# Kernel tuning notes

Measured on AMD Instinct MI355X. Metric: run time of the kernel, lower is better.

## Reference

```python
import jax, jax.numpy as jnp
import numpy as np

B, S, D = 8, 1024, 768
H, HD = 12, 64  # heads, head dim (H*HD == D)
EPS = 1e-12


def setup_inputs() -> dict:
    key = jax.random.key(0)
    ks = jax.random.split(key, 8)
    s = 0.02
    return {
        "hidden_states": jax.random.normal(ks[0], (B, S, D), jnp.float32),
        "attention_mask": jnp.zeros((B, 1, 1, S), jnp.float32),
        "head_mask": jnp.ones((H,), jnp.float32),
        "Wq": jax.random.normal(ks[1], (D, H * HD), jnp.float32) * s,
        "bq": jnp.zeros((H * HD,), jnp.float32),
        "Wk": jax.random.normal(ks[2], (D, H * HD), jnp.float32) * s,
        "bk": jnp.zeros((H * HD,), jnp.float32),
        "Wv": jax.random.normal(ks[3], (D, H * HD), jnp.float32) * s,
        "bv": jnp.zeros((H * HD,), jnp.float32),
        "Wo": jax.random.normal(ks[4], (D, H * HD), jnp.float32) * s,  # torch Linear weight [out=D, in=H*HD]
        "bo": jnp.zeros((D,), jnp.float32),
        "gamma": jnp.ones((D,), jnp.float32),
        "beta": jnp.zeros((D,), jnp.float32),
    }


def reference(hidden_states, attention_mask, head_mask, Wq, bq, Wk, bk, Wv, bv, Wo, bo, gamma, beta):
    def heads(x):  # [B,S,H*HD] -> [B,H,S,HD]
        return x.reshape(B, S, H, HD).transpose(0, 2, 1, 3)

    q = heads(hidden_states @ Wq.T + bq)
    k = heads(hidden_states @ Wk.T + bk)
    v = heads(hidden_states @ Wv.T + bv)

    scores = jnp.einsum("bhqd,bhkd->bhqk", q, k) / np.sqrt(HD).astype(np.float32)
    scores = scores + attention_mask
    probs = jax.nn.softmax(scores, axis=-1)  # dropout p=0 (eval)
    ctx = jnp.einsum("bhqk,bhkd->bhqd", probs, v)  # [B,H,S,HD]

    # masked per-head output projection: Wo.T.view(H, HD, D)
    Wph = Wo.T.reshape(H, HD, D)
    proj = jnp.einsum("bhsd,hde,h->bse", ctx, Wph, head_mask) + bo

    # residual + LayerNorm
    x = proj + hidden_states
    mu = jnp.mean(x, axis=-1, keepdims=True)
    var = jnp.mean(jnp.square(x - mu), axis=-1, keepdims=True)
    out = (x - mu) * jax.lax.rsqrt(var + EPS) * gamma + beta
    return out
```

## Files before the change

kernel.cpp:

```cpp
#include <hip/hip_runtime.h>
#include <hip/hip_bf16.h>
#include <math.h>

#define Bn 8
#define Sn 1024
#define Dn 768
#define Hn 12
#define MROWS (Bn * Sn)

typedef __attribute__((ext_vector_type(8))) short short8;
typedef __attribute__((ext_vector_type(4))) float floatx4;

__device__ __forceinline__ unsigned short f2b(float x) {
    union { float f; unsigned u; } v; v.f = x;
    unsigned r = v.u + 0x7fffu + ((v.u >> 16) & 1u);
    return (unsigned short)(r >> 16);
}

__device__ __forceinline__ unsigned pk2(float a, float b) {
    union { __hip_bfloat162 h; unsigned u; } v;
    v.h = __float22bfloat162_rn(float2{a, b});
    return v.u;
}

__device__ __forceinline__ float fexp2(float x) {
    float r;
    asm("v_exp_f32 %0, %1" : "=v"(r) : "v"(x));
    return r;
}

__device__ __forceinline__ void gload16(const void* g, void* l) {
    __builtin_amdgcn_global_load_lds(
        (const __attribute__((address_space(1))) void*)g,
        (__attribute__((address_space(3))) void*)l, 16, 0, 0);
}

#define MEMFENCE() asm volatile("" ::: "memory")
#define WAITV3()  asm volatile("s_waitcnt vmcnt(3)" ::: "memory")
#define WAITV0()  asm volatile("s_waitcnt vmcnt(0)" ::: "memory")
#define WAITLGKM() asm volatile("s_waitcnt lgkmcnt(0)" ::: "memory")


__global__ __launch_bounds__(256) void convert_all(const float* __restrict__ X,
                                                   const float* __restrict__ Wq, const float* __restrict__ Wk,
                                                   const float* __restrict__ Wv, const float* __restrict__ Wo,
                                                   unsigned short* __restrict__ Xb,
                                                   unsigned short* __restrict__ Wqb, unsigned short* __restrict__ Wkb,
                                                   unsigned short* __restrict__ Wvb, unsigned short* __restrict__ Wob) {
    const int id = blockIdx.x;
    const float* src;
    unsigned short* dst;
    int i;
    if (id < 6144) {
        src = X; dst = Xb;
        i = id * 256 + threadIdx.x;
    } else {
        const int y = (id - 6144) / 576;
        src = (y == 0) ? Wq : (y == 1) ? Wk : (y == 2) ? Wv : Wo;
        dst = (y == 0) ? Wqb : (y == 1) ? Wkb : (y == 2) ? Wvb : Wob;
        i = ((id - 6144) % 576) * 256 + threadIdx.x;
    }
    float4 v = reinterpret_cast<const float4*>(src)[i];
    ushort4 o;
    o.x = f2b(v.x); o.y = f2b(v.y); o.z = f2b(v.z); o.w = f2b(v.w);
    reinterpret_cast<ushort4*>(dst)[i] = o;
}

#define QKV_STAGE(t, b)                                                        \
    {                                                                          \
        const int k0 = (t) * 32;                                               \
        gload16(gAsrc[0] + k0, lAdst[0] + (b) * 8192);                         \
        gload16(gAsrc[1] + k0, lAdst[1] + (b) * 8192);                         \
        gload16(gWsrc + k0, lWdst + (b) * 4096);                               \
    }

#define QKV_COMP(b)                                                            \
    {                                                                          \
        const unsigned short* Ab = &As[b][0];                                  \
        const unsigned short* Wb = &Ws[b][0];                                  \
        short8 bf[4];                                                          \
        _Pragma("unroll") for (int j = 0; j < 4; j++)                          \
            bf[j] = *(const short8*)&Wb[woff[j]];                              \
        __builtin_amdgcn_s_setprio(1);                                         \
        _Pragma("unroll") for (int i = 0; i < 4; i++) {                        \
            short8 af = *(const short8*)&Ab[aoff[i]];                          \
            _Pragma("unroll") for (int j = 0; j < 4; j++)                      \
                acc[i][j] = __builtin_amdgcn_mfma_f32_16x16x32_bf16(           \
                    af, bf[j], acc[i][j], 0, 0, 0);                            \
        }                                                                      \
        __builtin_amdgcn_s_setprio(0);                                         \
    }

__global__ __launch_bounds__(512, 4) void gemm_qkv(const unsigned short* __restrict__ A,
                                                   const unsigned short* __restrict__ Wq,
                                                   const unsigned short* __restrict__ Wk,
                                                   const unsigned short* __restrict__ Wv,
                                                   const float* __restrict__ bq,
                                                   const float* __restrict__ bk,
                                                   const float* __restrict__ bv,
                                                   unsigned short* __restrict__ Qh,
                                                   unsigned short* __restrict__ Kh,
                                                   unsigned short* __restrict__ Vt) {
    __shared__ __align__(16) unsigned short As[3][256 * 32];
    __shared__ __align__(16) unsigned short Ws[3][128 * 32];
    const int orig = blockIdx.x;
    const int chunk = orig & 7;
    const int local = orig >> 3;
    const int by = chunk * 4 + local / 18;
    const int bxr = local % 18;
    const int mat = bxr / 6;
    const int m0 = by * 256;
    const int n0 = (bxr % 6) * 128;
    const unsigned short* W = (mat == 0) ? Wq : (mat == 1) ? Wk : Wv;
    const float* bias = (mat == 0) ? bq : (mat == 1) ? bk : bv;
    unsigned short* Cout = (mat == 0) ? Qh : (mat == 1) ? Kh : Vt;

    const int tid = threadIdx.x;
    const int w = tid >> 6, l = tid & 63, quad = l >> 4, mr = l & 15;
    const int wm = (w >> 1) * 64;
    const int wn = (w & 1) * 64;

    const unsigned short* gAsrc[2];
    unsigned short* lAdst[2];
#pragma unroll
    for (int j = 0; j < 2; j++) {
        const int u = tid + j * 512;
        const int r = u >> 2, c = u & 3;
        const int cp = c ^ ((r >> 1) & 3);
        gAsrc[j] = &A[(size_t)(m0 + r) * Dn + cp * 8];
        lAdst[j] = &As[0][u * 8];
    }
    const unsigned short* gWsrc;
    unsigned short* lWdst;
    {
        const int u = tid;
        const int r = u >> 2, c = u & 3;
        const int cp = c ^ ((r >> 1) & 3);
        gWsrc = &W[(size_t)(n0 + r) * Dn + cp * 8];
        lWdst = &Ws[0][u * 8];
    }

    int aoff[4], woff[4];
#pragma unroll
    for (int i = 0; i < 4; i++) {
        const int ra = wm + i * 16 + mr;
        aoff[i] = (ra * 4 + (quad ^ ((ra >> 1) & 3))) * 8;
    }
#pragma unroll
    for (int j = 0; j < 4; j++) {
        const int rw = wn + j * 16 + mr;
        woff[j] = (rw * 4 + (quad ^ ((rw >> 1) & 3))) * 8;
    }

    floatx4 acc[4][4];
#pragma unroll
    for (int i = 0; i < 4; i++)
#pragma unroll
        for (int j = 0; j < 4; j++) {
            floatx4 z = {0.f, 0.f, 0.f, 0.f};
            acc[i][j] = z;
        }

    QKV_STAGE(0, 0);
    QKV_STAGE(1, 1);

    for (int t = 0; t < 21; t += 3) {
        WAITV3();
        __builtin_amdgcn_s_barrier();
        MEMFENCE();
        QKV_STAGE(t + 2, 2);
        QKV_COMP(0);

        WAITV3();
        __builtin_amdgcn_s_barrier();
        MEMFENCE();
        QKV_STAGE(t + 3, 0);
        QKV_COMP(1);

        WAITV3();
        __builtin_amdgcn_s_barrier();
        MEMFENCE();
        QKV_STAGE(t + 4, 1);
        QKV_COMP(2);
    }
    WAITV3();
    __builtin_amdgcn_s_barrier();
    MEMFENCE();
    QKV_STAGE(23, 2);
    QKV_COMP(0);

    WAITV3();
    __builtin_amdgcn_s_barrier();
    MEMFENCE();
    QKV_COMP(1);

    WAITV0();
    __builtin_amdgcn_s_barrier();
    MEMFENCE();
    QKV_COMP(2);

#pragma unroll
    for (int j = 0; j < 4; j++) {
        const int col = n0 + wn + j * 16 + mr;
        const float bval = bias[col];
        const int h = col >> 6, d = col & 63;
#pragma unroll
        for (int i = 0; i < 4; i++) {
            const int mbase = m0 + wm + i * 16 + quad * 4;
            const int b = mbase >> 10, s0 = mbase & 1023;
            const size_t base = (size_t)(b * Hn + h) << 16;
            if (mat == 2) {
                ushort4 o;
                o.x = f2b(acc[i][j][0] + bval);
                o.y = f2b(acc[i][j][1] + bval);
                o.z = f2b(acc[i][j][2] + bval);
                o.w = f2b(acc[i][j][3] + bval);
                *reinterpret_cast<ushort4*>(&Cout[base + (size_t)d * 1024 + s0]) = o;
            } else {
#pragma unroll
                for (int r = 0; r < 4; r++) {
                    const float val = acc[i][j][r] + bval;
                    Cout[base + (size_t)(s0 + r) * 64 + d] = f2b(val);
                }
            }
        }
    }
}

#define OUT_STAGE(t, b)                                                        \
    {                                                                          \
        const int k0 = (t) * 32;                                               \
        gload16(gAsrc + k0, lAdst + (b) * 2048);                               \
        gload16(gWsrc[0] + k0, lWdst[0] + (b) * 4096);                         \
        gload16(gWsrc[1] + k0, lWdst[1] + (b) * 4096);                         \
    }

#define OUT_COMP(b)                                                            \
    {                                                                          \
        const unsigned short* Ab = &As[b][0];                                  \
        const unsigned short* Wb = &Ws[b][0];                                  \
        short8 bf[2];                                                          \
        _Pragma("unroll") for (int j = 0; j < 2; j++)                          \
            bf[j] = *(const short8*)&Wb[woff[j]];                              \
        __builtin_amdgcn_s_setprio(1);                                         \
        _Pragma("unroll") for (int i = 0; i < 4; i++) {                        \
            short8 af = *(const short8*)&Ab[aoff[i]];                          \
            _Pragma("unroll") for (int j = 0; j < 2; j++)                      \
                acc[i][j] = __builtin_amdgcn_mfma_f32_16x16x32_bf16(           \
                    af, bf[j], acc[i][j], 0, 0, 0);                            \
        }                                                                      \
        __builtin_amdgcn_s_setprio(0);                                         \
    }

__global__ __launch_bounds__(256, 4) void gemm_out(const unsigned short* __restrict__ A,
                                                   const unsigned short* __restrict__ W,
                                                   const float* __restrict__ bias,
                                                   const float* __restrict__ X,
                                                   float* __restrict__ xres) {
    __shared__ __align__(16) unsigned short As[3][64 * 32];
    __shared__ __align__(16) unsigned short Ws[3][128 * 32];
    const int id = blockIdx.x;
    const int by = id & 127;
    const int bx = id >> 7;
    const int m0 = by * 64;
    const int n0 = bx * 128;

    const int tid = threadIdx.x;
    const int w = tid >> 6, l = tid & 63, quad = l >> 4, mr = l & 15;

    const unsigned short* gAsrc;
    unsigned short* lAdst;
    {
        const int u = tid;
        const int r = u >> 2, c = u & 3;
        const int cp = c ^ ((r >> 1) & 3);
        gAsrc = &A[(size_t)(m0 + r) * Dn + cp * 8];
        lAdst = &As[0][u * 8];
    }
    const unsigned short* gWsrc[2];
    unsigned short* lWdst[2];
#pragma unroll
    for (int j = 0; j < 2; j++) {
        const int u = tid + j * 256;
        const int r = u >> 2, c = u & 3;
        const int cp = c ^ ((r >> 1) & 3);
        gWsrc[j] = &W[(size_t)(n0 + r) * Dn + cp * 8];
        lWdst[j] = &Ws[0][u * 8];
    }

    int aoff[4], woff[2];
#pragma unroll
    for (int i = 0; i < 4; i++) {
        const int ra = i * 16 + mr;
        aoff[i] = (ra * 4 + (quad ^ ((ra >> 1) & 3))) * 8;
    }
#pragma unroll
    for (int j = 0; j < 2; j++) {
        const int rw = w * 32 + j * 16 + mr;
        woff[j] = (rw * 4 + (quad ^ ((rw >> 1) & 3))) * 8;
    }

    floatx4 acc[4][2];
#pragma unroll
    for (int i = 0; i < 4; i++)
#pragma unroll
        for (int j = 0; j < 2; j++) {
            floatx4 z = {0.f, 0.f, 0.f, 0.f};
            acc[i][j] = z;
        }

    OUT_STAGE(0, 0);
    OUT_STAGE(1, 1);

    for (int t = 0; t < 21; t += 3) {
        WAITV3();
        __builtin_amdgcn_s_barrier();
        MEMFENCE();
        OUT_STAGE(t + 2, 2);
        OUT_COMP(0);

        WAITV3();
        __builtin_amdgcn_s_barrier();
        MEMFENCE();
        OUT_STAGE(t + 3, 0);
        OUT_COMP(1);

        WAITV3();
        __builtin_amdgcn_s_barrier();
        MEMFENCE();
        OUT_STAGE(t + 4, 1);
        OUT_COMP(2);
    }
    WAITV3();
    __builtin_amdgcn_s_barrier();
    MEMFENCE();
    OUT_STAGE(23, 2);
    OUT_COMP(0);

    WAITV3();
    __builtin_amdgcn_s_barrier();
    MEMFENCE();
    OUT_COMP(1);

    WAITV0();
    __builtin_amdgcn_s_barrier();
    MEMFENCE();
    OUT_COMP(2);

#pragma unroll
    for (int j = 0; j < 2; j++) {
        const int col = n0 + w * 32 + j * 16 + mr;
        const float bval = bias[col];
#pragma unroll
        for (int i = 0; i < 4; i++) {
#pragma unroll
            for (int r = 0; r < 4; r++) {
                const int m = m0 + i * 16 + quad * 4 + r;
                xres[(size_t)m * Dn + col] = acc[i][j][r] + bval + X[(size_t)m * Dn + col];
            }
        }
    }
}

__global__ __launch_bounds__(256) void flash_attn_mfma(const unsigned short* __restrict__ Qh,
                                                       const unsigned short* __restrict__ Kh,
                                                       const unsigned short* __restrict__ Vt,
                                                       const float* __restrict__ mask,
                                                       const float* __restrict__ head_mask,
                                                       unsigned short* __restrict__ ctx) {
    __shared__ __align__(16) unsigned short Ks[64 * 72];
    __shared__ __align__(16) unsigned short Vs[64 * 72];
    __shared__ __align__(16) unsigned short Ps[128 * 72];
    __shared__ float msk[64];

    const float LOG2E = 1.44269504088896f;
    const float C1 = 0.125f * 1.44269504088896f;

    const int id = blockIdx.x;
    const int bh = id % 96;
    const int qt = id / 96;
    const int b = bh / Hn, h = bh % Hn;
    const int q0 = qt * 128;
    const int tid = threadIdx.x;
    const int w = tid >> 6, l = tid & 63, quad = l >> 4, mr = l & 15;
    const size_t hb = (size_t)(b * Hn + h) << 16;

    short8 aq[2][2];
#pragma unroll
    for (int j = 0; j < 2; j++)
#pragma unroll
        for (int ks = 0; ks < 2; ks++)
            aq[j][ks] = *(const short8*)&Qh[hb + (size_t)(q0 + w * 32 + j * 16 + mr) * 64 + ks * 32 + quad * 8];

    float l_s[2] = {0.f, 0.f};
    floatx4 oacc[2][4];
#pragma unroll
    for (int i = 0; i < 2; i++)
#pragma unroll
        for (int jj = 0; jj < 4; jj++) {
            floatx4 z = {0.f, 0.f, 0.f, 0.f};
            oacc[i][jj] = z;
        }

    const int srow = tid >> 2;
    const int scol = (tid & 3) * 16;

    short8 pk0 = *(const short8*)&Kh[hb + (size_t)srow * 64 + scol];
    short8 pk1 = *(const short8*)&Kh[hb + (size_t)srow * 64 + scol + 8];
    short8 pv0 = *(const short8*)&Vt[hb + (size_t)srow * 1024 + scol];
    short8 pv1 = *(const short8*)&Vt[hb + (size_t)srow * 1024 + scol + 8];
    float pm = mask[b * Sn + (tid & 63)];

    for (int kt = 0; kt < Sn / 64; kt++) {
        __builtin_amdgcn_s_barrier();
        MEMFENCE();
        *(short8*)&Ks[srow * 72 + scol] = pk0;
        *(short8*)&Ks[srow * 72 + scol + 8] = pk1;
        *(short8*)&Vs[srow * 72 + scol] = pv0;
        *(short8*)&Vs[srow * 72 + scol + 8] = pv1;
        if (tid < 64) msk[tid] = pm * LOG2E;
        if (kt < Sn / 64 - 1) {
            const int k0 = (kt + 1) * 64;
            pk0 = *(const short8*)&Kh[hb + (size_t)(k0 + srow) * 64 + scol];
            pk1 = *(const short8*)&Kh[hb + (size_t)(k0 + srow) * 64 + scol + 8];
            pv0 = *(const short8*)&Vt[hb + (size_t)srow * 1024 + k0 + scol];
            pv1 = *(const short8*)&Vt[hb + (size_t)srow * 1024 + k0 + scol + 8];
            pm = mask[b * Sn + k0 + (tid & 63)];
        }
        WAITLGKM();
        __builtin_amdgcn_s_barrier();
        MEMFENCE();

        floatx4 sacc[4][2];
#pragma unroll
        for (int i = 0; i < 4; i++)
#pragma unroll
            for (int j = 0; j < 2; j++) {
                floatx4 z = {0.f, 0.f, 0.f, 0.f};
                sacc[i][j] = z;
            }
#pragma unroll
        for (int ks = 0; ks < 2; ks++) {
            short8 kfr[4];
#pragma unroll
            for (int i = 0; i < 4; i++)
                kfr[i] = *(const short8*)&Ks[(i * 16 + mr) * 72 + ks * 32 + quad * 8];
            __builtin_amdgcn_s_setprio(1);
#pragma unroll
            for (int i = 0; i < 4; i++)
#pragma unroll
                for (int j = 0; j < 2; j++)
                    sacc[i][j] = __builtin_amdgcn_mfma_f32_16x16x32_bf16(kfr[i], aq[j][ks], sacc[i][j], 0, 0, 0);
            __builtin_amdgcn_s_setprio(0);
        }

#pragma unroll
        for (int i = 0; i < 4; i++) {
            floatx4 mk4 = *(const floatx4*)&msk[i * 16 + quad * 4];
#pragma unroll
            for (int j = 0; j < 2; j++) {
                float p[4];
#pragma unroll
                for (int r = 0; r < 4; r++) {
                    p[r] = fexp2(sacc[i][j][r] * C1 + mk4[r]);
                    l_s[j] += p[r];
                }
                uint2 w2;
                w2.x = pk2(p[0], p[1]);
                w2.y = pk2(p[2], p[3]);
                *(uint2*)&Ps[(w * 32 + j * 16 + mr) * 72 + i * 16 + quad * 4] = w2;
            }
        }

#pragma unroll
        for (int ks = 0; ks < 2; ks++) {
            short8 ap0 = *(const short8*)&Ps[(w * 32 + mr) * 72 + ks * 32 + quad * 8];
            short8 ap1 = *(const short8*)&Ps[(w * 32 + 16 + mr) * 72 + ks * 32 + quad * 8];
            __builtin_amdgcn_s_setprio(1);
#pragma unroll
            for (int jj = 0; jj < 4; jj++) {
                short8 bv = *(const short8*)&Vs[(jj * 16 + mr) * 72 + ks * 32 + quad * 8];
                oacc[0][jj] = __builtin_amdgcn_mfma_f32_16x16x32_bf16(ap0, bv, oacc[0][jj], 0, 0, 0);
                oacc[1][jj] = __builtin_amdgcn_mfma_f32_16x16x32_bf16(ap1, bv, oacc[1][jj], 0, 0, 0);
            }
            __builtin_amdgcn_s_setprio(0);
        }
    }

    float L[2];
#pragma unroll
    for (int j = 0; j < 2; j++) {
        float t = l_s[j];
        t += __shfl_xor(t, 16);
        t += __shfl_xor(t, 32);
        L[j] = t;
    }
    const float hm = head_mask[h];
    float inv[2][4];
#pragma unroll
    for (int i = 0; i < 2; i++)
#pragma unroll
        for (int r = 0; r < 4; r++)
            inv[i][r] = hm / __shfl(L[i], quad * 4 + r);

#pragma unroll
    for (int i = 0; i < 2; i++)
#pragma unroll
        for (int jj = 0; jj < 4; jj++)
#pragma unroll
            for (int r = 0; r < 4; r++) {
                const int qrow = q0 + w * 32 + i * 16 + quad * 4 + r;
                ctx[(size_t)(b * Sn + qrow) * Dn + h * 64 + jj * 16 + mr] = f2b(oacc[i][jj][r] * inv[i][r]);
            }
}

__global__ __launch_bounds__(256) void ln_kernel(const float* __restrict__ x,
                                                 const float* __restrict__ gamma,
                                                 const float* __restrict__ beta,
                                                 float* __restrict__ out) {
    __shared__ float r1[4];
    __shared__ float r2[4];
    const int m = blockIdx.x;
    const int tid = threadIdx.x;
    const int w = tid >> 6, lane = tid & 63;

    float xv[3];
    float s = 0.f, ss = 0.f;
#pragma unroll
    for (int i = 0; i < 3; i++) {
        int j = tid + i * 256;
        float t = x[(size_t)m * Dn + j];
        xv[i] = t;
        s += t;
        ss += t * t;
    }
#pragma unroll
    for (int o = 1; o < 64; o <<= 1) {
        s += __shfl_xor(s, o);
        ss += __shfl_xor(ss, o);
    }
    if (lane == 0) { r1[w] = s; r2[w] = ss; }
    __syncthreads();
    const float sum = r1[0] + r1[1] + r1[2] + r1[3];
    const float sqs = r2[0] + r2[1] + r2[2] + r2[3];
    const float mu = sum * (1.0f / Dn);
    const float var = sqs * (1.0f / Dn) - mu * mu;
    const float rstd = rsqrtf(var + 1e-12f);
#pragma unroll
    for (int i = 0; i < 3; i++) {
        int j = tid + i * 256;
        out[(size_t)m * Dn + j] = (xv[i] - mu) * rstd * gamma[j] + beta[j];
    }
}

extern "C" void kernel_launch(void* const* d_in, const int* in_sizes, int n_in,
                              void* d_out, int out_size, void* d_ws, size_t ws_size,
                              hipStream_t stream) {
    const float* X         = (const float*)d_in[0];
    const float* mask      = (const float*)d_in[1];
    const float* head_mask = (const float*)d_in[2];
    const float* Wq        = (const float*)d_in[3];
    const float* bq        = (const float*)d_in[4];
    const float* Wk        = (const float*)d_in[5];
    const float* bk        = (const float*)d_in[6];
    const float* Wv        = (const float*)d_in[7];
    const float* bv        = (const float*)d_in[8];
    const float* Wo        = (const float*)d_in[9];
    const float* bo        = (const float*)d_in[10];
    const float* gamma     = (const float*)d_in[11];
    const float* beta      = (const float*)d_in[12];
    float* out = (float*)d_out;

    const size_t NE = (size_t)Bn * Sn * Dn;
    const size_t NW = (size_t)Dn * Dn;

    char* p = (char*)d_ws;
    unsigned short* Xb  = (unsigned short*)p;  p += NE * 2;
    unsigned short* Wqb = (unsigned short*)p;  p += NW * 2;
    unsigned short* Wkb = (unsigned short*)p;  p += NW * 2;
    unsigned short* Wvb = (unsigned short*)p;  p += NW * 2;
    unsigned short* Wob = (unsigned short*)p;  p += NW * 2;
    unsigned short* Qh  = (unsigned short*)p;  p += NE * 2;
    unsigned short* Kh  = (unsigned short*)p;  p += NE * 2;
    unsigned short* Vtb = (unsigned short*)p;  p += NE * 2;
    unsigned short* ctx = (unsigned short*)p;  p += NE * 2;
    float* xres = (float*)p;

    convert_all<<<8448, 256, 0, stream>>>(X, Wq, Wk, Wv, Wo, Xb, Wqb, Wkb, Wvb, Wob);

    gemm_qkv<<<576, 512, 0, stream>>>(Xb, Wqb, Wkb, Wvb, bq, bk, bv, Qh, Kh, Vtb);

    flash_attn_mfma<<<768, 256, 0, stream>>>(Qh, Kh, Vtb, mask, head_mask, ctx);

    gemm_out<<<768, 256, 0, stream>>>(ctx, Wob, bo, X, xres);

    ln_kernel<<<MROWS, 256, 0, stream>>>(xres, gamma, beta, out);
}
```

Before: 220.9 us.

## Shrink QKV GEMM tile to 128x128 with 256-thread blocks

Changes the QKV projection GEMM from 256x128 tiles on 512-thread blocks to 128x128 tiles on 256-thread blocks, doubling the grid to 1152 blocks. It also drops the chunked block-index swizzle in favour of a plain row-major mapping, and adjusts the load staging and vmcnt waits to four loads per stage. The aim is more blocks and better wave balance across CUs, at the cost of less reuse of the weight tile per block and possibly worse L2 locality without the swizzle.

Result: no change. 216.9 us (-1.8%).

```diff
diff --git a/kernel.cpp b/kernel.cpp
--- a/kernel.cpp
+++ b/kernel.cpp
@@ -36,6 +36,7 @@
 }
 
 #define MEMFENCE() asm volatile("" ::: "memory")
+#define WAITV4()  asm volatile("s_waitcnt vmcnt(4)" ::: "memory")
 #define WAITV3()  asm volatile("s_waitcnt vmcnt(3)" ::: "memory")
 #define WAITV0()  asm volatile("s_waitcnt vmcnt(0)" ::: "memory")
 #define WAITLGKM() asm volatile("s_waitcnt lgkmcnt(0)" ::: "memory")
@@ -69,9 +70,10 @@
 #define QKV_STAGE(t, b)                                                        \
     {                                                                          \
         const int k0 = (t) * 32;                                               \
-        gload16(gAsrc[0] + k0, lAdst[0] + (b) * 8192);                         \
-        gload16(gAsrc[1] + k0, lAdst[1] + (b) * 8192);                         \
-        gload16(gWsrc + k0, lWdst + (b) * 4096);                               \
+        gload16(gAsrc[0] + k0, lAdst[0] + (b) * 4096);                         \
+        gload16(gAsrc[1] + k0, lAdst[1] + (b) * 4096);                         \
+        gload16(gWsrc[0] + k0, lWdst[0] + (b) * 4096);                         \
+        gload16(gWsrc[1] + k0, lWdst[1] + (b) * 4096);                         \
     }
 
 #define QKV_COMP(b)                                                            \
@@ -91,7 +93,7 @@
         __builtin_amdgcn_s_setprio(0);                                         \
     }
 
-__global__ __launch_bounds__(512, 4) void gemm_qkv(const unsigned short* __restrict__ A,
+__global__ __launch_bounds__(256, 3) void gemm_qkv(const unsigned short* __restrict__ A,
                                                    const unsigned short* __restrict__ Wq,
                                                    const unsigned short* __restrict__ Wk,
                                                    const unsigned short* __restrict__ Wv,
@@ -101,43 +103,35 @@
                                                    unsigned short* __restrict__ Qh,
                                                    unsigned short* __restrict__ Kh,
                                                    unsigned short* __restrict__ Vt) {
-    __shared__ __align__(16) unsigned short As[3][256 * 32];
+    __shared__ __align__(16) unsigned short As[3][128 * 32];
     __shared__ __align__(16) unsigned short Ws[3][128 * 32];
-    const int orig = blockIdx.x;
-    const int chunk = orig & 7;
-    const int local = orig >> 3;
-    const int by = chunk * 4 + local / 18;
-    const int bxr = local % 18;
-    const int mat = bxr / 6;
-    const int m0 = by * 256;
-    const int n0 = (bxr % 6) * 128;
+    const int id = blockIdx.x;
+    const int by = id & 63;
+    const int bx = id >> 6;
+    const int mat = bx / 6;
+    const int m0 = by * 128;
+    const int n0 = (bx % 6) * 128;
     const unsigned short* W = (mat == 0) ? Wq : (mat == 1) ? Wk : Wv;
     const float* bias = (mat == 0) ? bq : (mat == 1) ? bk : bv;
     unsigned short* Cout = (mat == 0) ? Qh : (mat == 1) ? Kh : Vt;
 
     const int tid = threadIdx.x;
     const int w = tid >> 6, l = tid & 63, quad = l >> 4, mr = l & 15;
-    const int wm = (w >> 1) * 64;
-    const int wn = (w & 1) * 64;
+    const int wm = (w >> 1) * 64, wn = (w & 1) * 64;
 
     const unsigned short* gAsrc[2];
+    const unsigned short* gWsrc[2];
     unsigned short* lAdst[2];
+    unsigned short* lWdst[2];
 #pragma unroll
     for (int j = 0; j < 2; j++) {
-        const int u = tid + j * 512;
+        const int u = tid + j * 256;
         const int r = u >> 2, c = u & 3;
         const int cp = c ^ ((r >> 1) & 3);
         gAsrc[j] = &A[(size_t)(m0 + r) * Dn + cp * 8];
+        gWsrc[j] = &W[(size_t)(n0 + r) * Dn + cp * 8];
         lAdst[j] = &As[0][u * 8];
-    }
-    const unsigned short* gWsrc;
-    unsigned short* lWdst;
-    {
-        const int u = tid;
-        const int r = u >> 2, c = u & 3;
-        const int cp = c ^ ((r >> 1) & 3);
-        gWsrc = &W[(size_t)(n0 + r) * Dn + cp * 8];
-        lWdst = &Ws[0][u * 8];
+        lWdst[j] = &Ws[0][u * 8];
     }
 
     int aoff[4], woff[4];
@@ -165,31 +159,31 @@
     QKV_STAGE(1, 1);
 
     for (int t = 0; t < 21; t += 3) {
-        WAITV3();
+        WAITV4();
         __builtin_amdgcn_s_barrier();
         MEMFENCE();
         QKV_STAGE(t + 2, 2);
         QKV_COMP(0);
 
-        WAITV3();
+        WAITV4();
         __builtin_amdgcn_s_barrier();
         MEMFENCE();
         QKV_STAGE(t + 3, 0);
         QKV_COMP(1);
 
-        WAITV3();
+        WAITV4();
         __builtin_amdgcn_s_barrier();
         MEMFENCE();
         QKV_STAGE(t + 4, 1);
         QKV_COMP(2);
     }
-    WAITV3();
+    WAITV4();
     __builtin_amdgcn_s_barrier();
     MEMFENCE();
     QKV_STAGE(23, 2);
     QKV_COMP(0);
 
-    WAITV3();
+    WAITV4();
     __builtin_amdgcn_s_barrier();
     MEMFENCE();
     QKV_COMP(1);
@@ -588,7 +582,7 @@
 
     convert_all<<<8448, 256, 0, stream>>>(X, Wq, Wk, Wv, Wo, Xb, Wqb, Wkb, Wvb, Wob);
 
-    gemm_qkv<<<576, 512, 0, stream>>>(Xb, Wqb, Wkb, Wvb, bq, bk, bv, Qh, Kh, Vtb);
+    gemm_qkv<<<1152, 256, 0, stream>>>(Xb, Wqb, Wkb, Wvb, bq, bk, bv, Qh, Kh, Vtb);
 
     flash_attn_mfma<<<768, 256, 0, stream>>>(Qh, Kh, Vtb, mask, head_mask, ctx);
 
```
